# Kernel tuning notes

Hardware: AMD Instinct MI355X
Metric: run time of the kernel (lower is better)

## Reference

```python
import jax, jax.numpy as jnp
import numpy as np

MAX_ITER = 20
TAU = 1.0

def setup_inputs() -> dict:
    key = jax.random.key(0)
    s = jax.random.normal(key, (256, 512, 512), dtype=jnp.float32)
    return {"s": s}

def reference(s):
    # Sinkhorn-Knopp in log space. With nrows=ncols=None and square input,
    # the per-batch loop in the original reduces to full-matrix normalization.
    # Even iterations normalize along the last axis (dim=1 of each 2D matrix),
    # odd iterations along the row axis.
    log_s = s / TAU
    for i in range(MAX_ITER):
        axis = 2 if i % 2 == 0 else 1
        log_s = log_s - jax.nn.logsumexp(log_s, axis=axis, keepdims=True)
    return jnp.exp(log_s)
```

## Files before the change

kernel.cpp:

```cpp
#include <hip/hip_runtime.h>
#include <hip/hip_fp16.h>

#define N 512
#define WAVES 16
#define BLOCK (WAVES * 64)
#define ROWS_PER_WAVE (N / WAVES)

__global__ __launch_bounds__(BLOCK, 1)
void sinkhorn_kernel(const float* __restrict__ A, float* __restrict__ Out) {
    __shared__ float swv[N];
    __shared__ float sinvS[N];
    __shared__ float spart[WAVES][N];

    const float* __restrict__ Ab = A   + (size_t)blockIdx.x * (N * N);
    float* __restrict__ Ob       = Out + (size_t)blockIdx.x * (N * N);
    __half* __restrict__ Eh      = (__half*)Ob;

    const int tid  = threadIdx.x;
    const int lane = tid & 63;
    const int wave = tid >> 6;

    {
        float t0=0.f,t1=0.f,t2=0.f,t3=0.f,t4=0.f,t5=0.f,t6=0.f,t7=0.f;
        #pragma unroll 4
        for (int k = 0; k < ROWS_PER_WAVE; ++k) {
            const int row = k * WAVES + wave;
            const float4* R = (const float4*)(Ab + (size_t)row * N);
            const float4 x0 = R[2 * lane];
            const float4 x1 = R[2 * lane + 1];

            const float e0 = __expf(x0.x), e1 = __expf(x0.y),
                        e2 = __expf(x0.z), e3 = __expf(x0.w);
            const float e4 = __expf(x1.x), e5 = __expf(x1.y),
                        e6 = __expf(x1.z), e7 = __expf(x1.w);

            float4 pk;
            ((__half2*)&pk)[0] = __floats2half2_rn(e0, e1);
            ((__half2*)&pk)[1] = __floats2half2_rn(e2, e3);
            ((__half2*)&pk)[2] = __floats2half2_rn(e4, e5);
            ((__half2*)&pk)[3] = __floats2half2_rn(e6, e7);
            ((float4*)(Eh + (size_t)row * N))[lane] = pk;

            float S = ((e0 + e1) + (e2 + e3)) + ((e4 + e5) + (e6 + e7));
            #pragma unroll
            for (int m = 1; m < 64; m <<= 1) S += __shfl_xor(S, m, 64);

            const float inv = 1.0f / S;
            if (lane == 0) sinvS[row] = inv;

            t0 += e0 * inv; t1 += e1 * inv; t2 += e2 * inv; t3 += e3 * inv;
            t4 += e4 * inv; t5 += e5 * inv; t6 += e6 * inv; t7 += e7 * inv;
        }
        ((float4*)spart[wave])[2 * lane]     = make_float4(t0, t1, t2, t3);
        ((float4*)spart[wave])[2 * lane + 1] = make_float4(t4, t5, t6, t7);
        __syncthreads();
        if (tid < N) {
            float s = 0.f;
            #pragma unroll
            for (int w = 0; w < WAVES; ++w) s += spart[w][tid];
            swv[tid] = 1.0f / s;
        }
        __syncthreads();
    }

    for (int pass = 1; pass < 10; ++pass) {
        const float4 wa = ((const float4*)swv)[2 * lane];
        const float4 wb = ((const float4*)swv)[2 * lane + 1];
        float t0=0.f,t1=0.f,t2=0.f,t3=0.f,t4=0.f,t5=0.f,t6=0.f,t7=0.f;

        #pragma unroll 8
        for (int k = 0; k < ROWS_PER_WAVE; ++k) {
            const int row = k * WAVES + wave;
            const float4 raw = ((const float4*)(Eh + (size_t)row * N))[lane];
            const __half2* h = (const __half2*)&raw;
            const float2 f01 = __half22float2(h[0]);
            const float2 f23 = __half22float2(h[1]);
            const float2 f45 = __half22float2(h[2]);
            const float2 f67 = __half22float2(h[3]);

            const float s01 = f01.x * wa.x + f01.y * wa.y;
            const float s23 = f23.x * wa.z + f23.y * wa.w;
            const float s45 = f45.x * wb.x + f45.y * wb.y;
            const float s67 = f67.x * wb.z + f67.y * wb.w;
            float S = (s01 + s23) + (s45 + s67);
            #pragma unroll
            for (int m = 1; m < 64; m <<= 1) S += __shfl_xor(S, m, 64);

            const float inv = 1.0f / S;
            if (lane == 0) sinvS[row] = inv;

            t0 += f01.x * inv; t1 += f01.y * inv;
            t2 += f23.x * inv; t3 += f23.y * inv;
            t4 += f45.x * inv; t5 += f45.y * inv;
            t6 += f67.x * inv; t7 += f67.y * inv;
        }

        ((float4*)spart[wave])[2 * lane]     = make_float4(t0, t1, t2, t3);
        ((float4*)spart[wave])[2 * lane + 1] = make_float4(t4, t5, t6, t7);
        __syncthreads();
        if (tid < N) {
            float s = 0.f;
            #pragma unroll
            for (int w = 0; w < WAVES; ++w) s += spart[w][tid];
            swv[tid] = 1.0f / s;
        }
        __syncthreads();
    }

    {
        const float4 w0 = ((const float4*)swv)[lane];
        const float4 w1 = ((const float4*)swv)[lane + 64];
        #pragma unroll 4
        for (int k = 0; k < ROWS_PER_WAVE; ++k) {
            const int row = k * WAVES + wave;
            const float4* R = (const float4*)(Ab + (size_t)row * N);
            float4*       W = (float4*)(Ob + (size_t)row * N);
            const float4 x0 = R[lane];
            const float4 x1 = R[lane + 64];
            const float c = sinvS[row];

            float4 o0, o1;
            o0.x = __expf(x0.x) * (c * w0.x);
            o0.y = __expf(x0.y) * (c * w0.y);
            o0.z = __expf(x0.z) * (c * w0.z);
            o0.w = __expf(x0.w) * (c * w0.w);
            o1.x = __expf(x1.x) * (c * w1.x);
            o1.y = __expf(x1.y) * (c * w1.y);
            o1.z = __expf(x1.z) * (c * w1.z);
            o1.w = __expf(x1.w) * (c * w1.w);

            W[lane]      = o0;
            W[lane + 64] = o1;
        }
    }
}

extern "C" void kernel_launch(void* const* d_in, const int* in_sizes, int n_in,
                              void* d_out, int out_size, void* d_ws, size_t ws_size,
                              hipStream_t stream) {
    const float* s = (const float*)d_in[0];
    float* out = (float*)d_out;
    const int nmat = in_sizes[0] / (N * N);
    sinkhorn_kernel<<<nmat, BLOCK, 0, stream>>>(s, out);
}
```

Baseline: 751.3 us.

## Keep part of the fp16 exp matrix in registers and LDS across passes

Splits each wave's 32 rows of the half-precision exponentiated matrix three ways: 12 rows stay in registers, 7 rows in shared memory, and the rest in the global scratch. The global scratch layout also changes to thread-contiguous, fully coalesced uint4 stores. This cuts the repeated L2/global reads of the whole matrix across the nine balancing passes. In exchange, register and LDS pressure rise sharply, with about 150KB of LDS and a 4-blocks launch bound that caps VGPRs, so spilling is a risk.

After: 2.525 ms. +236.1%, slower.

```diff
diff --git a/kernel.cpp b/kernel.cpp
--- a/kernel.cpp
+++ b/kernel.cpp
@@ -4,52 +4,84 @@
 #define N 512
 #define WAVES 16
 #define BLOCK (WAVES * 64)
-#define ROWS_PER_WAVE (N / WAVES)
+#define RPW   (N / WAVES)
+#define REG_K 12
+#define LDS_K 7
+#define GLB_K (RPW - REG_K - LDS_K)
 
-__global__ __launch_bounds__(BLOCK, 1)
+
+#define PASS0_ROW(k, U0, U1, U2, U3) {                                        \
+    const int row = (k) * WAVES + wave;                                       \
+    const float4* R = (const float4*)(Ab + (size_t)row * N);                  \
+    const float4 x0 = R[2 * lane];                                            \
+    const float4 x1 = R[2 * lane + 1];                                        \
+    const float e0 = __expf(x0.x), e1 = __expf(x0.y),                         \
+                e2 = __expf(x0.z), e3 = __expf(x0.w);                         \
+    const float e4 = __expf(x1.x), e5 = __expf(x1.y),                         \
+                e6 = __expf(x1.z), e7 = __expf(x1.w);                         \
+    __half2 h01 = __floats2half2_rn(e0, e1), h23 = __floats2half2_rn(e2, e3); \
+    __half2 h45 = __floats2half2_rn(e4, e5), h67 = __floats2half2_rn(e6, e7); \
+    U0 = *(const unsigned*)&h01; U1 = *(const unsigned*)&h23;                 \
+    U2 = *(const unsigned*)&h45; U3 = *(const unsigned*)&h67;                 \
+    float S = ((e0 + e1) + (e2 + e3)) + ((e4 + e5) + (e6 + e7));              \
+    _Pragma("unroll") for (int m = 1; m < 64; m <<= 1)                        \
+        S += __shfl_xor(S, m, 64);                                            \
+    const float inv = 1.0f / S;                                               \
+    if (lane == 0) sinvS[row] = inv;                                          \
+    t0 += e0 * inv; t1 += e1 * inv; t2 += e2 * inv; t3 += e3 * inv;           \
+    t4 += e4 * inv; t5 += e5 * inv; t6 += e6 * inv; t7 += e7 * inv; }
+
+#define SWEEP_ROW(k, U0, U1, U2, U3) {                                        \
+    const int row = (k) * WAVES + wave;                                       \
+    const float2 f01 = __half22float2(*(const __half2*)&(U0));                \
+    const float2 f23 = __half22float2(*(const __half2*)&(U1));                \
+    const float2 f45 = __half22float2(*(const __half2*)&(U2));                \
+    const float2 f67 = __half22float2(*(const __half2*)&(U3));                \
+    const float s01 = f01.x * wa.x + f01.y * wa.y;                            \
+    const float s23 = f23.x * wa.z + f23.y * wa.w;                            \
+    const float s45 = f45.x * wb.x + f45.y * wb.y;                            \
+    const float s67 = f67.x * wb.z + f67.y * wb.w;                            \
+    float S = (s01 + s23) + (s45 + s67);                                      \
+    _Pragma("unroll") for (int m = 1; m < 64; m <<= 1)                        \
+        S += __shfl_xor(S, m, 64);                                            \
+    const float inv = 1.0f / S;                                               \
+    if (lane == 0) sinvS[row] = inv;                                          \
+    t0 += f01.x * inv; t1 += f01.y * inv;                                     \
+    t2 += f23.x * inv; t3 += f23.y * inv;                                     \
+    t4 += f45.x * inv; t5 += f45.y * inv;                                     \
+    t6 += f67.x * inv; t7 += f67.y * inv; }
+
+__global__ __launch_bounds__(BLOCK, 4)
 void sinkhorn_kernel(const float* __restrict__ A, float* __restrict__ Out) {
     __shared__ float swv[N];
     __shared__ float sinvS[N];
     __shared__ float spart[WAVES][N];
+    __shared__ uint4 Esh[LDS_K * BLOCK];
 
     const float* __restrict__ Ab = A   + (size_t)blockIdx.x * (N * N);
     float* __restrict__ Ob       = Out + (size_t)blockIdx.x * (N * N);
-    __half* __restrict__ Eh      = (__half*)Ob;
+    uint4* __restrict__ Eg       = (uint4*)Ob;
 
     const int tid  = threadIdx.x;
     const int lane = tid & 63;
     const int wave = tid >> 6;
 
+    unsigned eR[REG_K][4];
+
     {
         float t0=0.f,t1=0.f,t2=0.f,t3=0.f,t4=0.f,t5=0.f,t6=0.f,t7=0.f;
-        #pragma unroll 4
-        for (int k = 0; k < ROWS_PER_WAVE; ++k) {
-            const int row = k * WAVES + wave;
-            const float4* R = (const float4*)(Ab + (size_t)row * N);
-            const float4 x0 = R[2 * lane];
-            const float4 x1 = R[2 * lane + 1];
-
-            const float e0 = __expf(x0.x), e1 = __expf(x0.y),
-                        e2 = __expf(x0.z), e3 = __expf(x0.w);
-            const float e4 = __expf(x1.x), e5 = __expf(x1.y),
-                        e6 = __expf(x1.z), e7 = __expf(x1.w);
-
-            float4 pk;
-            ((__half2*)&pk)[0] = __floats2half2_rn(e0, e1);
-            ((__half2*)&pk)[1] = __floats2half2_rn(e2, e3);
-            ((__half2*)&pk)[2] = __floats2half2_rn(e4, e5);
-            ((__half2*)&pk)[3] = __floats2half2_rn(e6, e7);
-            ((float4*)(Eh + (size_t)row * N))[lane] = pk;
-
-            float S = ((e0 + e1) + (e2 + e3)) + ((e4 + e5) + (e6 + e7));
-            #pragma unroll
-            for (int m = 1; m < 64; m <<= 1) S += __shfl_xor(S, m, 64);
-
-            const float inv = 1.0f / S;
-            if (lane == 0) sinvS[row] = inv;
-
-            t0 += e0 * inv; t1 += e1 * inv; t2 += e2 * inv; t3 += e3 * inv;
-            t4 += e4 * inv; t5 += e5 * inv; t6 += e6 * inv; t7 += e7 * inv;
+        #pragma unroll
+        for (int k = 0; k < REG_K; ++k)
+            PASS0_ROW(k, eR[k][0], eR[k][1], eR[k][2], eR[k][3]);
+        #pragma unroll
+        for (int k = REG_K; k < REG_K + LDS_K; ++k) {
+            unsigned u0,u1,u2,u3; PASS0_ROW(k, u0,u1,u2,u3);
+            Esh[(k - REG_K) * BLOCK + tid] = make_uint4(u0,u1,u2,u3);
+        }
+        #pragma unroll 2
+        for (int k = REG_K + LDS_K; k < RPW; ++k) {
+            unsigned u0,u1,u2,u3; PASS0_ROW(k, u0,u1,u2,u3);
+            Eg[(size_t)(k - REG_K - LDS_K) * BLOCK + tid] = make_uint4(u0,u1,u2,u3);
         }
         ((float4*)spart[wave])[2 * lane]     = make_float4(t0, t1, t2, t3);
         ((float4*)spart[wave])[2 * lane + 1] = make_float4(t4, t5, t6, t7);
@@ -68,31 +100,18 @@
         const float4 wb = ((const float4*)swv)[2 * lane + 1];
         float t0=0.f,t1=0.f,t2=0.f,t3=0.f,t4=0.f,t5=0.f,t6=0.f,t7=0.f;
 
-        #pragma unroll 8
-        for (int k = 0; k < ROWS_PER_WAVE; ++k) {
-            const int row = k * WAVES + wave;
-            const float4 raw = ((const float4*)(Eh + (size_t)row * N))[lane];
-            const __half2* h = (const __half2*)&raw;
-            const float2 f01 = __half22float2(h[0]);
-            const float2 f23 = __half22float2(h[1]);
-            const float2 f45 = __half22float2(h[2]);
-            const float2 f67 = __half22float2(h[3]);
-
-            const float s01 = f01.x * wa.x + f01.y * wa.y;
-            const float s23 = f23.x * wa.z + f23.y * wa.w;
-            const float s45 = f45.x * wb.x + f45.y * wb.y;
-            const float s67 = f67.x * wb.z + f67.y * wb.w;
-            float S = (s01 + s23) + (s45 + s67);
-            #pragma unroll
-            for (int m = 1; m < 64; m <<= 1) S += __shfl_xor(S, m, 64);
-
-            const float inv = 1.0f / S;
-            if (lane == 0) sinvS[row] = inv;
-
-            t0 += f01.x * inv; t1 += f01.y * inv;
-            t2 += f23.x * inv; t3 += f23.y * inv;
-            t4 += f45.x * inv; t5 += f45.y * inv;
-            t6 += f67.x * inv; t7 += f67.y * inv;
+        #pragma unroll 2
+        for (int k = REG_K + LDS_K; k < RPW; ++k) {
+            const uint4 g = Eg[(size_t)(k - REG_K - LDS_K) * BLOCK + tid];
+            SWEEP_ROW(k, g.x, g.y, g.z, g.w);
+        }
+        #pragma unroll
+        for (int k = 0; k < REG_K; ++k)
+            SWEEP_ROW(k, eR[k][0], eR[k][1], eR[k][2], eR[k][3]);
+        #pragma unroll
+        for (int k = REG_K; k < REG_K + LDS_K; ++k) {
+            const uint4 g = Esh[(k - REG_K) * BLOCK + tid];
+            SWEEP_ROW(k, g.x, g.y, g.z, g.w);
         }
 
         ((float4*)spart[wave])[2 * lane]     = make_float4(t0, t1, t2, t3);
@@ -111,7 +130,7 @@
         const float4 w0 = ((const float4*)swv)[lane];
         const float4 w1 = ((const float4*)swv)[lane + 64];
         #pragma unroll 4
-        for (int k = 0; k < ROWS_PER_WAVE; ++k) {
+        for (int k = 0; k < RPW; ++k) {
             const int row = k * WAVES + wave;
             const float4* R = (const float4*)(Ab + (size_t)row * N);
             float4*       W = (float4*)(Ob + (size_t)row * N);
```
